# Performance work log

Hardware: AMD Instinct MI355X
Metric: run time of the kernel (lower is better)

The kernel has to match this reference:

```python
import jax, jax.numpy as jnp
import numpy as np

B, N, F, E, H, A, V, L = 128, 196, 512, 512, 512, 512, 30000, 21


def setup_inputs() -> dict:
    key = jax.random.key(0)
    ks = jax.random.split(key, 20)
    s = 0.02
    d = {
        "feats": jax.random.normal(ks[0], (B, N, F), jnp.float32),
        "captions": jax.random.randint(ks[1], (B, L), 1, V),
        "embed_W": (jax.random.normal(ks[2], (V, E), jnp.float32) * s).at[0].set(0.0),
        "Wf_w": jax.random.normal(ks[3], (A, F), jnp.float32) * s,
        "Wf_b": jnp.zeros((A,), jnp.float32),
        "Wh_w": jax.random.normal(ks[4], (A, H), jnp.float32) * s,
        "Wh_b": jnp.zeros((A,), jnp.float32),
        "v_w": jax.random.normal(ks[5], (1, A), jnp.float32) * s,
        "v_b": jnp.zeros((1,), jnp.float32),
        "W_ih": jax.random.normal(ks[6], (4 * H, E + F), jnp.float32) * s,
        "W_hh": jax.random.normal(ks[7], (4 * H, H), jnp.float32) * s,
        "b_ih": jnp.zeros((4 * H,), jnp.float32),
        "b_hh": jnp.zeros((4 * H,), jnp.float32),
        "init_w": jax.random.normal(ks[8], (H, F), jnp.float32) * s,
        "init_b": jnp.zeros((H,), jnp.float32),
        "initc_w": jax.random.normal(ks[9], (H, F), jnp.float32) * s,
        "initc_b": jnp.zeros((H,), jnp.float32),
        "out_w": jax.random.normal(ks[10], (V, H), jnp.float32) * s,
        "out_b": jnp.zeros((V,), jnp.float32),
    }
    return d


def reference(feats, captions, embed_W, Wf_w, Wf_b, Wh_w, Wh_b, v_w, v_b,
              W_ih, W_hh, b_ih, b_hh, init_w, init_b, initc_w, initc_b,
              out_w, out_b):
    # padding_idx=0 -> embedding row 0 is zero
    emW = embed_W.at[0].set(0.0)
    emb = emW[captions[:, :-1]]                       # [B, T, E], T = L-1
    gfeat = feats.mean(axis=1)                        # [B, F]
    h0 = gfeat @ init_w.T + init_b                    # [B, H]
    c0 = gfeat @ initc_w.T + initc_b                  # [B, H]
    # attention feature projection is timestep-invariant: hoist out of loop
    fproj = jnp.einsum('bnf,af->bna', feats, Wf_w) + Wf_b  # [B, N, A]

    def step(carry, emb_t):
        h, c = carry
        hproj = h @ Wh_w.T + Wh_b                     # [B, A]
        e = jnp.tanh(fproj + hproj[:, None, :])       # [B, N, A]
        scores = jnp.einsum('bna,a->bn', e, v_w[0]) + v_b[0]
        w = jax.nn.softmax(scores, axis=1)            # [B, N]
        ctx = jnp.einsum('bnf,bn->bf', feats, w)      # [B, F]
        x = jnp.concatenate([emb_t, ctx], axis=1)     # [B, E+F]
        gates = x @ W_ih.T + b_ih + h @ W_hh.T + b_hh # [B, 4H]
        i, f, g, o = jnp.split(gates, 4, axis=1)      # torch gate order i,f,g,o
        i = jax.nn.sigmoid(i)
        f = jax.nn.sigmoid(f)
        g = jnp.tanh(g)
        o = jax.nn.sigmoid(o)
        c = f * c + i * g
        h = o * jnp.tanh(c)
        logit = h @ out_w.T + out_b                   # [B, V]
        return (h, c), logit

    _, logits = jax.lax.scan(step, (h0, c0), jnp.swapaxes(emb, 0, 1))
    return jnp.swapaxes(logits, 0, 1)                 # [B, T, V]
```

## Files before the change

### kernel.cpp

```cpp
#include <hip/hip_runtime.h>
#include <stdint.h>
#include <stddef.h>

typedef unsigned short u16;
typedef __attribute__((ext_vector_type(8))) short short8;
typedef __attribute__((ext_vector_type(4))) float f32x4;

#define DEV static __device__ __forceinline__

DEV float bf2f(u16 u){ return __uint_as_float(((unsigned)u)<<16); }
DEV u16 f2bf(float f){ unsigned x=__float_as_uint(f); return (u16)((x + 0x7fffu + ((x>>16)&1u))>>16); }

DEV float wsum(float v){
#pragma unroll
  for(int o=32;o;o>>=1) v += __shfl_xor(v,o);
  return v;
}
DEV float wmax(float v){
#pragma unroll
  for(int o=32;o;o>>=1) v = fmaxf(v,__shfl_xor(v,o));
  return v;
}
DEV float sigm(float x){ return __fdividef(1.f, 1.f+__expf(-x)); }
DEV float tanhx(float x){ float e=__expf(-2.f*fabsf(x)); float t=__fdividef(1.f-e,1.f+e); return x<0.f?-t:t; }

DEV f32x4 mfma16(short8 a, short8 b, f32x4 c){
  asm("v_mfma_f32_16x16x32_bf16 %0, %1, %2, %0" : "+v"(c) : "v"(a), "v"(b));
  return c;
}
DEV void gll16(const void* g, void* l){
  __builtin_amdgcn_global_load_lds((const __attribute__((address_space(1))) void*)g,
                                   (__attribute__((address_space(3))) void*)l, 16, 0, 0);
}

DEV void pack8(u16* dst, const float* src){
  const float4 a=*(const float4*)(src);
  const float4 b=*(const float4*)(src+4);
  short8 o;
  o[0]=(short)f2bf(a.x); o[1]=(short)f2bf(a.y); o[2]=(short)f2bf(a.z); o[3]=(short)f2bf(a.w);
  o[4]=(short)f2bf(b.x); o[5]=(short)f2bf(b.y); o[6]=(short)f2bf(b.z); o[7]=(short)f2bf(b.w);
  *(short8*)dst=o;
}
DEV void zero8(u16* dst){
  short8 z;
#pragma unroll
  for(int e=0;e<8;++e) z[e]=0;
  *(short8*)dst=z;
}

__global__ __launch_bounds__(256) void setup_cast(
  const float* __restrict__ feats, const int* __restrict__ captions,
  const float* __restrict__ embW, const float* __restrict__ Wf_w,
  const float* __restrict__ Wh_w, const float* __restrict__ W_ih,
  const float* __restrict__ W_hh, const float* __restrict__ b_ih,
  const float* __restrict__ b_hh, const float* __restrict__ out_w,
  u16* __restrict__ feats_bf, u16* __restrict__ outw_bf, u16* __restrict__ Wc,
  u16* __restrict__ WihE, u16* __restrict__ embx, u16* __restrict__ Whw_bf,
  u16* __restrict__ Wf_bf, float* __restrict__ bias_comb)
{
  const long long o0=12845056LL,o1=28246016LL,o2=30343168LL,o3=31391744LL,
                  o4=32702464LL,o5=32964608LL,o6=33226752LL,total=33228800LL;
  for (long long i8=((long long)blockIdx.x*256+threadIdx.x)*8; i8<total;
       i8+=(long long)gridDim.x*256*8){
    const long long i=i8;
    if (i<o0){ pack8(feats_bf+i, feats+i); }
    else if (i<o1){ const long long j=i-o0; const int r=(int)(j>>9);
      if (r<30000) pack8(outw_bf+j, out_w+j); else zero8(outw_bf+j); }
    else if (i<o2){ const long long j=i-o1; const int r=(int)(j>>10), k=(int)(j&1023);
      const int o=((r&3)<<9)+(r>>2);
      const float* s=(k<512)? (W_ih+(size_t)o*1024+512+k) : (W_hh+(size_t)o*512+(k-512));
      pack8(Wc+j, s); }
    else if (i<o3){ const long long j=i-o2; const int r=(int)(j>>9), k=(int)(j&511);
      const int o=((r&3)<<9)+(r>>2);
      pack8(WihE+j, W_ih+(size_t)o*1024+k); }
    else if (i<o4){ const long long j=i-o3; const int m=(int)(j>>9), e=(int)(j&511);
      const int b=m/20, tt=m-b*20; const int idx=captions[b*21+tt];
      if (idx) pack8(embx+j, embW+(size_t)idx*512+e); else zero8(embx+j); }
    else if (i<o5){ const long long j=i-o4; pack8(Whw_bf+j, Wh_w+j); }
    else if (i<o6){ const long long j=i-o5; pack8(Wf_bf+j, Wf_w+j); }
    else { const long long j=i-o6;
      for(int e=0;e<8;++e){ const int r=(int)(j+e); const int o=((r&3)<<9)+(r>>2);
        bias_comb[r]=b_ih[o]+b_hh[o]; } }
  }
}

__global__ __launch_bounds__(256) void prep(
  const float* __restrict__ feats, const float* __restrict__ init_w,
  const float* __restrict__ init_b, const float* __restrict__ initc_w,
  const float* __restrict__ initc_b, u16* __restrict__ xs0, float* __restrict__ cbuf)
{
  const int b=blockIdx.x, tid=threadIdx.x, lane=tid&63, w=tid>>6;
  __shared__ float gf[512];
  const float* fb=feats+(size_t)b*196*512;
  float a0=0.f,a1=0.f;
  for(int n=0;n<196;++n){ a0+=fb[(size_t)n*512+tid]; a1+=fb[(size_t)n*512+tid+256]; }
  gf[tid]=a0*(1.f/196.f); gf[tid+256]=a1*(1.f/196.f);
  __syncthreads();
  const int kb=lane*8;
  float g8[8];
#pragma unroll
  for(int e=0;e<8;++e) g8[e]=gf[kb+e];
  for(int j=w*128;j<w*128+128;++j){
    const float* r1=init_w+(size_t)j*512+kb;
    const float* r2=initc_w+(size_t)j*512+kb;
    float s1=0.f,s2=0.f;
#pragma unroll
    for(int e=0;e<8;++e){ s1+=g8[e]*r1[e]; s2+=g8[e]*r2[e]; }
    s1=wsum(s1); s2=wsum(s2);
    if(lane==(j&63)){ xs0[b*1024+512+j]=f2bf(s1+init_b[j]); cbuf[b*512+j]=s2+initc_b[j]; }
  }
}

__global__ __launch_bounds__(1024) void attn_step(
  const u16* __restrict__ fproj, const u16* __restrict__ feats_bf,
  u16* __restrict__ xs, const u16* __restrict__ Whw,
  const float* __restrict__ Whb, const float* __restrict__ vw,
  const float* __restrict__ vb, const float* __restrict__ gemb,
  const float* __restrict__ gpart, float* __restrict__ cbuf,
  u16* __restrict__ h_all, int t)
{
  const int b=blockIdx.x, tid=threadIdx.x, lane=tid&63, w=tid>>6;
  __shared__ float part[16][512];
  __shared__ float hsf[512], hp[512], sc[208], red[16];
  if (t>0){
    if (tid<512){
      const int u=tid;
      float4 g4=*(const float4*)&gemb[((size_t)b*20+(t-1))*2048+u*4];
#pragma unroll
      for(int kz=0;kz<4;++kz){
        const float4 p=*(const float4*)&gpart[((size_t)kz*128+b)*2048+u*4];
        g4.x+=p.x; g4.y+=p.y; g4.z+=p.z; g4.w+=p.w;
      }
      const float cn=sigm(g4.y)*cbuf[b*512+u]+sigm(g4.x)*tanhx(g4.z);
      const float hn=sigm(g4.w)*tanhx(cn);
      cbuf[b*512+u]=cn;
      const u16 hb=f2bf(hn);
      xs[b*1024+512+u]=hb;
      h_all[((size_t)b*20+(t-1))*512+u]=hb;
      hsf[u]=bf2f(hb);
    }
  } else {
    if (tid<512) hsf[tid]=bf2f(xs[b*1024+512+tid]);
  }
  __syncthreads();
  const int kb=lane*8;
  float h8[8];
#pragma unroll
  for(int e=0;e<8;++e) h8[e]=hsf[kb+e];
  for(int jj=0;jj<32;jj+=2){
    const int j=w*32+jj;
    short8 w0=*(const short8*)(Whw+(size_t)j*512+kb);
    short8 w1=*(const short8*)(Whw+(size_t)(j+1)*512+kb);
    float s0=0.f,s1=0.f;
#pragma unroll
    for(int e=0;e<8;++e){
      s0+=h8[e]*bf2f((u16)w0[e]);
      s1+=h8[e]*bf2f((u16)w1[e]);
    }
    s0=wsum(s0); s1=wsum(s1);
    if(lane==0){ hp[j]=s0+Whb[j]; hp[j+1]=s1+Whb[j+1]; }
  }
  __syncthreads();
  float p2[8], vm2[8];
  float sv=0.f;
#pragma unroll
  for(int e=0;e<8;++e){
    const float p=hp[kb+e], v=vw[kb+e];
    p2[e]=2.f*p; vm2[e]=-2.f*v; sv+=v;
  }
  const float vb0=vb[0];
#pragma unroll
  for(int i=0;i<12;i+=2){
    const int n0=w+16*i, n1=n0+16;
    short8 f0=*(const short8*)(fproj+((size_t)b*196+n0)*512+kb);
    short8 f1=*(const short8*)(fproj+((size_t)b*196+n1)*512+kb);
    float s0=sv, s1=sv;
#pragma unroll
    for(int e=0;e<8;++e){
      const float x0=fmaf(bf2f((u16)f0[e]),2.f,p2[e]);
      const float x1=fmaf(bf2f((u16)f1[e]),2.f,p2[e]);
      s0+=__fdividef(vm2[e],__expf(x0)+1.f);
      s1+=__fdividef(vm2[e],__expf(x1)+1.f);
    }
    s0=wsum(s0); s1=wsum(s1);
    if(lane==0){ sc[n0]=s0+vb0; sc[n1]=s1+vb0; }
  }
  {
    const int n=w+192;
    if (n<196){
      short8 f0=*(const short8*)(fproj+((size_t)b*196+n)*512+kb);
      float s0=sv;
#pragma unroll
      for(int e=0;e<8;++e){
        const float x0=fmaf(bf2f((u16)f0[e]),2.f,p2[e]);
        s0+=__fdividef(vm2[e],__expf(x0)+1.f);
      }
      s0=wsum(s0);
      if(lane==0) sc[n]=s0+vb0;
    }
  }
  __syncthreads();
  float xv=(tid<196)? sc[tid] : -3.0e38f;
  float mx=wmax(xv);
  if(lane==0) red[w]=mx;
  __syncthreads();
  float mm=red[0];
#pragma unroll
  for(int i=1;i<16;++i) mm=fmaxf(mm,red[i]);
  float pv=(tid<196)? __expf(xv-mm) : 0.f;
  float ps=wsum(pv);
  __syncthreads();
  if(lane==0) red[w]=ps;
  __syncthreads();
  float tot=red[0];
#pragma unroll
  for(int i=1;i<16;++i) tot+=red[i];
  if(tid<196) sc[tid]=__fdividef(pv,tot);
  __syncthreads();
  float a8[8];
#pragma unroll
  for(int e=0;e<8;++e) a8[e]=0.f;
  for(int n=w;n<196;n+=16){
    short8 fv=*(const short8*)(feats_bf+((size_t)b*196+n)*512+kb);
    const float wn=sc[n];
#pragma unroll
    for(int e=0;e<8;++e) a8[e]+=wn*bf2f((u16)fv[e]);
  }
  *(float4*)&part[w][kb]  =*(float4*)&a8[0];
  *(float4*)&part[w][kb+4]=*(float4*)&a8[4];
  __syncthreads();
  if (tid<512){
    float s=0.f;
#pragma unroll
    for(int i=0;i<16;++i) s+=part[i][tid];
    xs[b*1024+tid]=f2bf(s);
  }
}

__global__ __launch_bounds__(512) void lstm_fin(
  const float* __restrict__ gemb, const float* __restrict__ gpart,
  const float* __restrict__ cbuf, u16* __restrict__ h_all)
{
  const int b=blockIdx.x, u=threadIdx.x;
  float4 g4=*(const float4*)&gemb[((size_t)b*20+19)*2048+u*4];
#pragma unroll
  for(int kz=0;kz<4;++kz){
    const float4 p=*(const float4*)&gpart[((size_t)kz*128+b)*2048+u*4];
    g4.x+=p.x; g4.y+=p.y; g4.z+=p.z; g4.w+=p.w;
  }
  const float cn=sigm(g4.y)*cbuf[b*512+u]+sigm(g4.x)*tanhx(g4.z);
  const float hn=sigm(g4.w)*tanhx(cn);
  h_all[((size_t)b*20+19)*512+u]=f2bf(hn);
}

template<int MODE>
__global__ __launch_bounds__(256) void gemm_bt(
  const u16* __restrict__ A, int lda, const u16* __restrict__ Bw, int ldb, int K,
  const float* __restrict__ bias, float* __restrict__ outf, u16* __restrict__ outb,
  int ncols)
{
  const int bm=(MODE==4)? 0 : blockIdx.y*128;
  const int kz=(MODE==4)? blockIdx.y : 0;
  const int bn=blockIdx.x*128;
  const u16* __restrict__ Ap=A +(size_t)kz*256;
  const u16* __restrict__ Bp=Bw+(size_t)kz*256;
  const int tid=threadIdx.x, lane=tid&63, wave=tid>>6;
  const int wr=(wave>>1)*64, wc=(wave&1)*64;
  __shared__ u16 As[128*32], Bs[128*32];
  f32x4 acc[4][4]={};
  const int srow=tid>>2, scol=(tid&3)*8;
  for(int k0=0;k0<K;k0+=32){
    gll16(Ap+(size_t)(bm+srow)*lda    +k0+scol, As+tid*8);
    gll16(Ap+(size_t)(bm+64+srow)*lda +k0+scol, As+2048+tid*8);
    gll16(Bp+(size_t)(bn+srow)*ldb    +k0+scol, Bs+tid*8);
    gll16(Bp+(size_t)(bn+64+srow)*ldb +k0+scol, Bs+2048+tid*8);
    __syncthreads();
    short8 af[4], bfr[4];
    const int ro=lane&15, ko=(lane>>4)*8;
#pragma unroll
    for(int m=0;m<4;++m) af[m]=*(const short8*)(As+(wr+m*16+ro)*32+ko);
#pragma unroll
    for(int n=0;n<4;++n) bfr[n]=*(const short8*)(Bs+(wc+n*16+ro)*32+ko);
#pragma unroll
    for(int m=0;m<4;++m)
#pragma unroll
      for(int n=0;n<4;++n) acc[m][n]=mfma16(af[m],bfr[n],acc[m][n]);
    __syncthreads();
  }
  asm volatile("s_nop 7\ns_nop 7\ns_nop 7");
  const int ro4=(lane>>4)*4, co=lane&15;
#pragma unroll
  for(int m=0;m<4;++m)
#pragma unroll
    for(int n=0;n<4;++n)
#pragma unroll
      for(int j=0;j<4;++j){
        const int r=bm+wr+m*16+ro4+j, c=bn+wc+n*16+co;
        if constexpr (MODE==0)      outb[(size_t)r*ncols+c]=f2bf(acc[m][n][j]+bias[c]);
        else if constexpr (MODE==1) outf[(size_t)r*ncols+c]=acc[m][n][j]+bias[c];
        else if constexpr (MODE==2){ if (c<ncols) outf[(size_t)r*ncols+c]=acc[m][n][j]+bias[c]; }
        else                        outf[((size_t)kz*128+r)*ncols+c]=acc[m][n][j];
      }
}

extern "C" void kernel_launch(void* const* d_in, const int* in_sizes, int n_in,
                              void* d_out, int out_size, void* d_ws, size_t ws_size,
                              hipStream_t stream) {
  const float* feats   =(const float*)d_in[0];
  const int*   captions=(const int*)  d_in[1];
  const float* embW    =(const float*)d_in[2];
  const float* Wf_w    =(const float*)d_in[3];
  const float* Wf_b    =(const float*)d_in[4];
  const float* Wh_w    =(const float*)d_in[5];
  const float* Wh_b    =(const float*)d_in[6];
  const float* v_w     =(const float*)d_in[7];
  const float* v_b     =(const float*)d_in[8];
  const float* W_ih    =(const float*)d_in[9];
  const float* W_hh    =(const float*)d_in[10];
  const float* b_ih    =(const float*)d_in[11];
  const float* b_hh    =(const float*)d_in[12];
  const float* init_w  =(const float*)d_in[13];
  const float* init_b  =(const float*)d_in[14];
  const float* initc_w =(const float*)d_in[15];
  const float* initc_b =(const float*)d_in[16];
  const float* out_w   =(const float*)d_in[17];
  const float* out_b   =(const float*)d_in[18];
  float* out=(float*)d_out;
  char* ws=(char*)d_ws;

  u16*   feats_bf =(u16*)  (ws+0);
  u16*   fproj    =(u16*)  (ws+25690112);
  u16*   outw_bf  =(u16*)  (ws+51380224);
  u16*   Wc       =(u16*)  (ws+82182144);
  u16*   WihE     =(u16*)  (ws+86376448);
  u16*   Whw_bf   =(u16*)  (ws+88473600);
  u16*   Wf_bf    =(u16*)  (ws+88997888);
  u16*   embx     =(u16*)  (ws+89522176);
  u16*   h_all    =(u16*)  (ws+92143616);
  u16*   xs0      =(u16*)  (ws+94765056);
  float* gemb     =(float*)(ws+95289344);
  float* cbuf     =(float*)(ws+116260864);
  float* bias_comb=(float*)(ws+116523008);
  float* gpart    =(float*)(ws+116531200);

  setup_cast<<<4096,256,0,stream>>>(feats,captions,embW,Wf_w,Wh_w,W_ih,W_hh,b_ih,b_hh,out_w,
                                    feats_bf,outw_bf,Wc,WihE,embx,Whw_bf,Wf_bf,bias_comb);
  prep<<<128,256,0,stream>>>(feats,init_w,init_b,initc_w,initc_b,xs0,cbuf);
  gemm_bt<0><<<dim3(4,196),256,0,stream>>>(feats_bf,512,Wf_bf,512,512,
      Wf_b,nullptr,fproj,512);
  gemm_bt<1><<<dim3(16,20),256,0,stream>>>(embx,512,WihE,512,512,
      bias_comb,gemb,nullptr,2048);

  for(int t=0;t<20;++t){
    attn_step<<<128,1024,0,stream>>>(fproj,feats_bf,xs0,Whw_bf,Wh_b,v_w,v_b,
                                     gemb,gpart,cbuf,h_all,t);
    gemm_bt<4><<<dim3(16,4),256,0,stream>>>(xs0,1024,Wc,1024,256,
        nullptr,gpart,nullptr,2048);
  }
  lstm_fin<<<128,512,0,stream>>>(gemb,gpart,cbuf,h_all);
  gemm_bt<2><<<dim3(235,20),256,0,stream>>>(h_all,512,outw_bf,512,512,
      out_b,out,nullptr,30000);
}
```

Measured before the change: 1.245 ms.

## Fuse recurrent timestep loop into one persistent kernel with grid barriers

Replaces the 20 pairs of attention and recurrent-GEMM launches plus the final LSTM kernel with a single persistent 128-block kernel that loops over timesteps. Blocks synchronise through a software grid barrier built on global atomics. The recurrent GEMM is redistributed so that each block computes a 128x128 tile with a split-K of 8 instead of 4. This removes about 40 launch boundaries, at the cost of two spin-wait grid barriers per step and a larger shared-memory footprint. It also relies on all 128 blocks being co-resident, which a plain launch does not guarantee.

```diff
diff --git a/kernel.cpp b/kernel.cpp
--- a/kernel.cpp
+++ b/kernel.cpp
@@ -46,6 +46,25 @@
 #pragma unroll
   for(int e=0;e<8;++e) z[e]=0;
   *(short8*)dst=z;
+}
+
+DEV void gbar(unsigned* cnt, unsigned* gen, int nblk){
+  __syncthreads();
+  if (threadIdx.x==0){
+    __threadfence();
+    unsigned g=__hip_atomic_load(gen,__ATOMIC_RELAXED,__HIP_MEMORY_SCOPE_AGENT);
+    unsigned a=__hip_atomic_fetch_add(cnt,1u,__ATOMIC_ACQ_REL,__HIP_MEMORY_SCOPE_AGENT);
+    if (a==(unsigned)(nblk-1)){
+      __hip_atomic_store(cnt,0u,__ATOMIC_RELAXED,__HIP_MEMORY_SCOPE_AGENT);
+      __hip_atomic_store(gen,g+1u,__ATOMIC_RELEASE,__HIP_MEMORY_SCOPE_AGENT);
+    } else {
+      while(__hip_atomic_load(gen,__ATOMIC_ACQUIRE,__HIP_MEMORY_SCOPE_AGENT)==g){
+        __builtin_amdgcn_s_sleep(1);
+      }
+    }
+    __threadfence();
+  }
+  __syncthreads();
 }
 
 __global__ __launch_bounds__(256) void setup_cast(
@@ -111,146 +130,189 @@
   }
 }
 
-__global__ __launch_bounds__(1024) void attn_step(
+__global__ __launch_bounds__(1024) void megastep(
   const u16* __restrict__ fproj, const u16* __restrict__ feats_bf,
   u16* __restrict__ xs, const u16* __restrict__ Whw,
   const float* __restrict__ Whb, const float* __restrict__ vw,
   const float* __restrict__ vb, const float* __restrict__ gemb,
-  const float* __restrict__ gpart, float* __restrict__ cbuf,
-  u16* __restrict__ h_all, int t)
+  float* __restrict__ gpart, float* __restrict__ cbuf,
+  u16* __restrict__ h_all, const u16* __restrict__ Wc,
+  unsigned* __restrict__ bar)
 {
-  const int b=blockIdx.x, tid=threadIdx.x, lane=tid&63, w=tid>>6;
+  const int blk=blockIdx.x, tid=threadIdx.x, lane=tid&63, w=tid>>6;
+  const int b=blk;
   __shared__ float part[16][512];
   __shared__ float hsf[512], hp[512], sc[208], red[16];
-  if (t>0){
-    if (tid<512){
-      const int u=tid;
-      float4 g4=*(const float4*)&gemb[((size_t)b*20+(t-1))*2048+u*4];
-#pragma unroll
-      for(int kz=0;kz<4;++kz){
-        const float4 p=*(const float4*)&gpart[((size_t)kz*128+b)*2048+u*4];
-        g4.x+=p.x; g4.y+=p.y; g4.z+=p.z; g4.w+=p.w;
-      }
-      const float cn=sigm(g4.y)*cbuf[b*512+u]+sigm(g4.x)*tanhx(g4.z);
-      const float hn=sigm(g4.w)*tanhx(cn);
-      cbuf[b*512+u]=cn;
-      const u16 hb=f2bf(hn);
-      xs[b*1024+512+u]=hb;
-      h_all[((size_t)b*20+(t-1))*512+u]=hb;
-      hsf[u]=bf2f(hb);
-    }
-  } else {
-    if (tid<512) hsf[tid]=bf2f(xs[b*1024+512+tid]);
-  }
-  __syncthreads();
+  __shared__ u16 As[128*128], Bs[128*128];
+  unsigned* cnt=bar; unsigned* gen=bar+1;
+
   const int kb=lane*8;
-  float h8[8];
-#pragma unroll
-  for(int e=0;e<8;++e) h8[e]=hsf[kb+e];
-  for(int jj=0;jj<32;jj+=2){
-    const int j=w*32+jj;
-    short8 w0=*(const short8*)(Whw+(size_t)j*512+kb);
-    short8 w1=*(const short8*)(Whw+(size_t)(j+1)*512+kb);
-    float s0=0.f,s1=0.f;
+  const int kz=blk>>4, nt=blk&15;
+
+  for (int t=0;t<20;++t){
+    if (t>0){
+      if (tid<512){
+        const int u=tid;
+        float4 g4=*(const float4*)&gemb[((size_t)b*20+(t-1))*2048+u*4];
+#pragma unroll
+        for(int z=0;z<8;++z){
+          const float4 p=*(const float4*)&gpart[((size_t)z*128+b)*2048+u*4];
+          g4.x+=p.x; g4.y+=p.y; g4.z+=p.z; g4.w+=p.w;
+        }
+        const float cn=sigm(g4.y)*cbuf[b*512+u]+sigm(g4.x)*tanhx(g4.z);
+        const float hn=sigm(g4.w)*tanhx(cn);
+        cbuf[b*512+u]=cn;
+        const u16 hb=f2bf(hn);
+        xs[b*1024+512+u]=hb;
+        h_all[((size_t)b*20+(t-1))*512+u]=hb;
+        hsf[u]=bf2f(hb);
+      }
+    } else {
+      if (tid<512) hsf[tid]=bf2f(xs[b*1024+512+tid]);
+    }
+    __syncthreads();
+    float h8[8];
+#pragma unroll
+    for(int e=0;e<8;++e) h8[e]=hsf[kb+e];
+    for(int jj=0;jj<32;jj+=2){
+      const int j=w*32+jj;
+      short8 w0=*(const short8*)(Whw+(size_t)j*512+kb);
+      short8 w1=*(const short8*)(Whw+(size_t)(j+1)*512+kb);
+      float s0=0.f,s1=0.f;
+#pragma unroll
+      for(int e=0;e<8;++e){
+        s0+=h8[e]*bf2f((u16)w0[e]);
+        s1+=h8[e]*bf2f((u16)w1[e]);
+      }
+      s0=wsum(s0); s1=wsum(s1);
+      if(lane==0){ hp[j]=s0+Whb[j]; hp[j+1]=s1+Whb[j+1]; }
+    }
+    __syncthreads();
+    float p2[8], vm2[8];
+    float sv=0.f;
 #pragma unroll
     for(int e=0;e<8;++e){
-      s0+=h8[e]*bf2f((u16)w0[e]);
-      s1+=h8[e]*bf2f((u16)w1[e]);
-    }
-    s0=wsum(s0); s1=wsum(s1);
-    if(lane==0){ hp[j]=s0+Whb[j]; hp[j+1]=s1+Whb[j+1]; }
-  }
-  __syncthreads();
-  float p2[8], vm2[8];
-  float sv=0.f;
-#pragma unroll
-  for(int e=0;e<8;++e){
-    const float p=hp[kb+e], v=vw[kb+e];
-    p2[e]=2.f*p; vm2[e]=-2.f*v; sv+=v;
-  }
-  const float vb0=vb[0];
-#pragma unroll
-  for(int i=0;i<12;i+=2){
-    const int n0=w+16*i, n1=n0+16;
-    short8 f0=*(const short8*)(fproj+((size_t)b*196+n0)*512+kb);
-    short8 f1=*(const short8*)(fproj+((size_t)b*196+n1)*512+kb);
-    float s0=sv, s1=sv;
-#pragma unroll
-    for(int e=0;e<8;++e){
-      const float x0=fmaf(bf2f((u16)f0[e]),2.f,p2[e]);
-      const float x1=fmaf(bf2f((u16)f1[e]),2.f,p2[e]);
-      s0+=__fdividef(vm2[e],__expf(x0)+1.f);
-      s1+=__fdividef(vm2[e],__expf(x1)+1.f);
-    }
-    s0=wsum(s0); s1=wsum(s1);
-    if(lane==0){ sc[n0]=s0+vb0; sc[n1]=s1+vb0; }
-  }
-  {
-    const int n=w+192;
-    if (n<196){
-      short8 f0=*(const short8*)(fproj+((size_t)b*196+n)*512+kb);
-      float s0=sv;
+      const float p=hp[kb+e], v=vw[kb+e];
+      p2[e]=2.f*p; vm2[e]=-2.f*v; sv+=v;
+    }
+    const float vb0=vb[0];
+#pragma unroll
+    for(int i=0;i<12;i+=2){
+      const int n0=w+16*i, n1=n0+16;
+      short8 f0=*(const short8*)(fproj+((size_t)b*196+n0)*512+kb);
+      short8 f1=*(const short8*)(fproj+((size_t)b*196+n1)*512+kb);
+      float s0=sv, s1=sv;
 #pragma unroll
       for(int e=0;e<8;++e){
         const float x0=fmaf(bf2f((u16)f0[e]),2.f,p2[e]);
+        const float x1=fmaf(bf2f((u16)f1[e]),2.f,p2[e]);
         s0+=__fdividef(vm2[e],__expf(x0)+1.f);
-      }
-      s0=wsum(s0);
-      if(lane==0) sc[n]=s0+vb0;
-    }
-  }
-  __syncthreads();
-  float xv=(tid<196)? sc[tid] : -3.0e38f;
-  float mx=wmax(xv);
-  if(lane==0) red[w]=mx;
-  __syncthreads();
-  float mm=red[0];
-#pragma unroll
-  for(int i=1;i<16;++i) mm=fmaxf(mm,red[i]);
-  float pv=(tid<196)? __expf(xv-mm) : 0.f;
-  float ps=wsum(pv);
-  __syncthreads();
-  if(lane==0) red[w]=ps;
-  __syncthreads();
-  float tot=red[0];
-#pragma unroll
-  for(int i=1;i<16;++i) tot+=red[i];
-  if(tid<196) sc[tid]=__fdividef(pv,tot);
-  __syncthreads();
-  float a8[8];
-#pragma unroll
-  for(int e=0;e<8;++e) a8[e]=0.f;
-  for(int n=w;n<196;n+=16){
-    short8 fv=*(const short8*)(feats_bf+((size_t)b*196+n)*512+kb);
-    const float wn=sc[n];
-#pragma unroll
-    for(int e=0;e<8;++e) a8[e]+=wn*bf2f((u16)fv[e]);
-  }
-  *(float4*)&part[w][kb]  =*(float4*)&a8[0];
-  *(float4*)&part[w][kb+4]=*(float4*)&a8[4];
-  __syncthreads();
+        s1+=__fdividef(vm2[e],__expf(x1)+1.f);
+      }
+      s0=wsum(s0); s1=wsum(s1);
+      if(lane==0){ sc[n0]=s0+vb0; sc[n1]=s1+vb0; }
+    }
+    {
+      const int n=w+192;
+      if (n<196){
+        short8 f0=*(const short8*)(fproj+((size_t)b*196+n)*512+kb);
+        float s0=sv;
+#pragma unroll
+        for(int e=0;e<8;++e){
+          const float x0=fmaf(bf2f((u16)f0[e]),2.f,p2[e]);
+          s0+=__fdividef(vm2[e],__expf(x0)+1.f);
+        }
+        s0=wsum(s0);
+        if(lane==0) sc[n]=s0+vb0;
+      }
+    }
+    __syncthreads();
+    float xv=(tid<196)? sc[tid] : -3.0e38f;
+    float mx=wmax(xv);
+    if(lane==0) red[w]=mx;
+    __syncthreads();
+    float mm=red[0];
+#pragma unroll
+    for(int i=1;i<16;++i) mm=fmaxf(mm,red[i]);
+    float pv=(tid<196)? __expf(xv-mm) : 0.f;
+    float ps=wsum(pv);
+    __syncthreads();
+    if(lane==0) red[w]=ps;
+    __syncthreads();
+    float tot=red[0];
+#pragma unroll
+    for(int i=1;i<16;++i) tot+=red[i];
+    if(tid<196) sc[tid]=__fdividef(pv,tot);
+    __syncthreads();
+    float a8[8];
+#pragma unroll
+    for(int e=0;e<8;++e) a8[e]=0.f;
+    for(int n=w;n<196;n+=16){
+      short8 fv=*(const short8*)(feats_bf+((size_t)b*196+n)*512+kb);
+      const float wn=sc[n];
+#pragma unroll
+      for(int e=0;e<8;++e) a8[e]+=wn*bf2f((u16)fv[e]);
+    }
+    *(float4*)&part[w][kb]  =*(float4*)&a8[0];
+    *(float4*)&part[w][kb+4]=*(float4*)&a8[4];
+    __syncthreads();
+    if (tid<512){
+      float s=0.f;
+#pragma unroll
+      for(int i=0;i<16;++i) s+=part[i][tid];
+      xs[b*1024+tid]=f2bf(s);
+    }
+
+    gbar(cnt,gen,128);
+
+#pragma unroll
+    for(int i=0;i<2;++i){
+      const int idx=i*1024+tid;
+      gll16(xs+(size_t)(idx>>4)*1024 + kz*128 + (idx&15)*8, As+idx*8);
+    }
+#pragma unroll
+    for(int i=0;i<2;++i){
+      const int idx=i*1024+tid;
+      gll16(Wc+(size_t)(nt*128+(idx>>4))*1024 + kz*128 + (idx&15)*8, Bs+idx*8);
+    }
+    __syncthreads();
+    {
+      f32x4 acc[4]={};
+      const int mf=w>>1, nc0=(w&1)*64, ro=lane&15, ko=(lane>>4)*8;
+#pragma unroll
+      for(int kk=0;kk<4;++kk){
+        short8 af=*(const short8*)(As+(size_t)(mf*16+ro)*128+kk*32+ko);
+#pragma unroll
+        for(int n=0;n<4;++n){
+          short8 bfv=*(const short8*)(Bs+(size_t)(nc0+n*16+ro)*128+kk*32+ko);
+          acc[n]=mfma16(af,bfv,acc[n]);
+        }
+      }
+      asm volatile("s_nop 7\ns_nop 7\ns_nop 7");
+      const int ro4=(lane>>4)*4, co=lane&15;
+#pragma unroll
+      for(int n=0;n<4;++n)
+#pragma unroll
+        for(int j=0;j<4;++j){
+          const int r=mf*16+ro4+j, c=nt*128+nc0+n*16+co;
+          gpart[((size_t)kz*128+r)*2048+c]=acc[n][j];
+        }
+    }
+    gbar(cnt,gen,128);
+  }
+
   if (tid<512){
-    float s=0.f;
-#pragma unroll
-    for(int i=0;i<16;++i) s+=part[i][tid];
-    xs[b*1024+tid]=f2bf(s);
-  }
-}
-
-__global__ __launch_bounds__(512) void lstm_fin(
-  const float* __restrict__ gemb, const float* __restrict__ gpart,
-  const float* __restrict__ cbuf, u16* __restrict__ h_all)
-{
-  const int b=blockIdx.x, u=threadIdx.x;
-  float4 g4=*(const float4*)&gemb[((size_t)b*20+19)*2048+u*4];
-#pragma unroll
-  for(int kz=0;kz<4;++kz){
-    const float4 p=*(const float4*)&gpart[((size_t)kz*128+b)*2048+u*4];
-    g4.x+=p.x; g4.y+=p.y; g4.z+=p.z; g4.w+=p.w;
-  }
-  const float cn=sigm(g4.y)*cbuf[b*512+u]+sigm(g4.x)*tanhx(g4.z);
-  const float hn=sigm(g4.w)*tanhx(cn);
-  h_all[((size_t)b*20+19)*512+u]=f2bf(hn);
+    const int u=tid;
+    float4 g4=*(const float4*)&gemb[((size_t)b*20+19)*2048+u*4];
+#pragma unroll
+    for(int z=0;z<8;++z){
+      const float4 p=*(const float4*)&gpart[((size_t)z*128+b)*2048+u*4];
+      g4.x+=p.x; g4.y+=p.y; g4.z+=p.z; g4.w+=p.w;
+    }
+    const float cn=sigm(g4.y)*cbuf[b*512+u]+sigm(g4.x)*tanhx(g4.z);
+    const float hn=sigm(g4.w)*tanhx(cn);
+    h_all[((size_t)b*20+19)*512+u]=f2bf(hn);
+  }
 }
 
 template<int MODE>
@@ -259,21 +321,17 @@
   const float* __restrict__ bias, float* __restrict__ outf, u16* __restrict__ outb,
   int ncols)
 {
-  const int bm=(MODE==4)? 0 : blockIdx.y*128;
-  const int kz=(MODE==4)? blockIdx.y : 0;
-  const int bn=blockIdx.x*128;
-  const u16* __restrict__ Ap=A +(size_t)kz*256;
-  const u16* __restrict__ Bp=Bw+(size_t)kz*256;
+  const int bm=blockIdx.y*128, bn=blockIdx.x*128;
   const int tid=threadIdx.x, lane=tid&63, wave=tid>>6;
   const int wr=(wave>>1)*64, wc=(wave&1)*64;
   __shared__ u16 As[128*32], Bs[128*32];
   f32x4 acc[4][4]={};
   const int srow=tid>>2, scol=(tid&3)*8;
   for(int k0=0;k0<K;k0+=32){
-    gll16(Ap+(size_t)(bm+srow)*lda    +k0+scol, As+tid*8);
-    gll16(Ap+(size_t)(bm+64+srow)*lda +k0+scol, As+2048+tid*8);
-    gll16(Bp+(size_t)(bn+srow)*ldb    +k0+scol, Bs+tid*8);
-    gll16(Bp+(size_t)(bn+64+srow)*ldb +k0+scol, Bs+2048+tid*8);
+    gll16(A +(size_t)(bm+srow)*lda    +k0+scol, As+tid*8);
+    gll16(A +(size_t)(bm+64+srow)*lda +k0+scol, As+2048+tid*8);
+    gll16(Bw+(size_t)(bn+srow)*ldb    +k0+scol, Bs+tid*8);
+    gll16(Bw+(size_t)(bn+64+srow)*ldb +k0+scol, Bs+2048+tid*8);
     __syncthreads();
     short8 af[4], bfr[4];
     const int ro=lane&15, ko=(lane>>4)*8;
@@ -298,8 +356,7 @@
         const int r=bm+wr+m*16+ro4+j, c=bn+wc+n*16+co;
         if constexpr (MODE==0)      outb[(size_t)r*ncols+c]=f2bf(acc[m][n][j]+bias[c]);
         else if constexpr (MODE==1) outf[(size_t)r*ncols+c]=acc[m][n][j]+bias[c];
-        else if constexpr (MODE==2){ if (c<ncols) outf[(size_t)r*ncols+c]=acc[m][n][j]+bias[c]; }
-        else                        outf[((size_t)kz*128+r)*ncols+c]=acc[m][n][j];
+        else { if (c<ncols) outf[(size_t)r*ncols+c]=acc[m][n][j]+bias[c]; }
       }
 }
 
@@ -342,7 +399,9 @@
   float* cbuf     =(float*)(ws+116260864);
   float* bias_comb=(float*)(ws+116523008);
   float* gpart    =(float*)(ws+116531200);
-
+  unsigned* bar   =(unsigned*)(ws+126000000);
+
+  hipMemsetAsync(bar, 0, 8, stream);
   setup_cast<<<4096,256,0,stream>>>(feats,captions,embW,Wf_w,Wh_w,W_ih,W_hh,b_ih,b_hh,out_w,
                                     feats_bf,outw_bf,Wc,WihE,embx,Whw_bf,Wf_bf,bias_comb);
   prep<<<128,256,0,stream>>>(feats,init_w,init_b,initc_w,initc_b,xs0,cbuf);
@@ -351,13 +410,9 @@
   gemm_bt<1><<<dim3(16,20),256,0,stream>>>(embx,512,WihE,512,512,
       bias_comb,gemb,nullptr,2048);
 
-  for(int t=0;t<20;++t){
-    attn_step<<<128,1024,0,stream>>>(fproj,feats_bf,xs0,Whw_bf,Wh_b,v_w,v_b,
-                                     gemb,gpart,cbuf,h_all,t);
-    gemm_bt<4><<<dim3(16,4),256,0,stream>>>(xs0,1024,Wc,1024,256,
-        nullptr,gpart,nullptr,2048);
-  }
-  lstm_fin<<<128,512,0,stream>>>(gemb,gpart,cbuf,h_all);
+  megastep<<<128,1024,0,stream>>>(fproj,feats_bf,xs0,Whw_bf,Wh_b,v_w,v_b,
+                                  gemb,gpart,cbuf,h_all,Wc,bar);
+
   gemm_bt<2><<<dim3(235,20),256,0,stream>>>(h_all,512,outw_bf,512,512,
       out_b,out,nullptr,30000);
 }
```

Measured after the change: 3.504 ms. +181.5%, slower.

## Split attention step into score and context kernels over two blocks per batch

Applied to the files above, without the earlier changes.

The per-batch 1024-thread attention kernel becomes two 512-thread kernels, each launched with two blocks per batch row. Each block owns half the attention positions or half the context features, so the 128-row recurrence fills more CUs. Scores now go through a global buffer and the cell state is double-buffered, because both half-blocks recompute the LSTM update and Wh projection redundantly. The output-projection GEMM grid is also transposed so consecutive blocks share the same weight tile, improving cache reuse. The price is an extra kernel launch per timestep plus duplicated projection work.

```diff
diff --git a/kernel.cpp b/kernel.cpp
--- a/kernel.cpp
+++ b/kernel.cpp
@@ -4,6 +4,7 @@
 
 typedef unsigned short u16;
 typedef __attribute__((ext_vector_type(8))) short short8;
+typedef __attribute__((ext_vector_type(4))) short short4v;
 typedef __attribute__((ext_vector_type(4))) float f32x4;
 
 #define DEV static __device__ __forceinline__
@@ -111,44 +112,43 @@
   }
 }
 
-__global__ __launch_bounds__(1024) void attn_step(
-  const u16* __restrict__ fproj, const u16* __restrict__ feats_bf,
-  u16* __restrict__ xs, const u16* __restrict__ Whw,
-  const float* __restrict__ Whb, const float* __restrict__ vw,
-  const float* __restrict__ vb, const float* __restrict__ gemb,
-  const float* __restrict__ gpart, float* __restrict__ cbuf,
-  u16* __restrict__ h_all, int t)
-{
-  const int b=blockIdx.x, tid=threadIdx.x, lane=tid&63, w=tid>>6;
-  __shared__ float part[16][512];
-  __shared__ float hsf[512], hp[512], sc[208], red[16];
+__global__ __launch_bounds__(512) void attn_sc(
+  const u16* __restrict__ fproj, u16* __restrict__ xs,
+  const u16* __restrict__ Whw, const float* __restrict__ Whb,
+  const float* __restrict__ vw, const float* __restrict__ vb,
+  const float* __restrict__ gemb, const float* __restrict__ gpart,
+  float* __restrict__ cbuf, u16* __restrict__ h_all,
+  float* __restrict__ sc_g, int t)
+{
+  const int blk=blockIdx.x, tid=threadIdx.x, lane=tid&63, w=tid>>6;
+  const int b=blk>>1, h=blk&1;
+  __shared__ float hsf[512], hp[512];
   if (t>0){
-    if (tid<512){
-      const int u=tid;
-      float4 g4=*(const float4*)&gemb[((size_t)b*20+(t-1))*2048+u*4];
-#pragma unroll
-      for(int kz=0;kz<4;++kz){
-        const float4 p=*(const float4*)&gpart[((size_t)kz*128+b)*2048+u*4];
-        g4.x+=p.x; g4.y+=p.y; g4.z+=p.z; g4.w+=p.w;
-      }
-      const float cn=sigm(g4.y)*cbuf[b*512+u]+sigm(g4.x)*tanhx(g4.z);
-      const float hn=sigm(g4.w)*tanhx(cn);
-      cbuf[b*512+u]=cn;
-      const u16 hb=f2bf(hn);
-      xs[b*1024+512+u]=hb;
-      h_all[((size_t)b*20+(t-1))*512+u]=hb;
-      hsf[u]=bf2f(hb);
-    }
+    const int u=tid;
+    float4 g4=*(const float4*)&gemb[((size_t)b*20+(t-1))*2048+u*4];
+#pragma unroll
+    for(int kz=0;kz<4;++kz){
+      const float4 p=*(const float4*)&gpart[((size_t)kz*128+b)*2048+u*4];
+      g4.x+=p.x; g4.y+=p.y; g4.z+=p.z; g4.w+=p.w;
+    }
+    const float cold=cbuf[((t-1)&1)*65536 + b*512+u];
+    const float cn=sigm(g4.y)*cold+sigm(g4.x)*tanhx(g4.z);
+    const float hn=sigm(g4.w)*tanhx(cn);
+    cbuf[(t&1)*65536 + b*512+u]=cn;
+    const u16 hb=f2bf(hn);
+    xs[b*1024+512+u]=hb;
+    h_all[((size_t)b*20+(t-1))*512+u]=hb;
+    hsf[u]=bf2f(hb);
   } else {
-    if (tid<512) hsf[tid]=bf2f(xs[b*1024+512+tid]);
+    hsf[tid]=bf2f(xs[b*1024+512+tid]);
   }
   __syncthreads();
   const int kb=lane*8;
   float h8[8];
 #pragma unroll
   for(int e=0;e<8;++e) h8[e]=hsf[kb+e];
-  for(int jj=0;jj<32;jj+=2){
-    const int j=w*32+jj;
+  for(int jj=0;jj<64;jj+=2){
+    const int j=w*64+jj;
     short8 w0=*(const short8*)(Whw+(size_t)j*512+kb);
     short8 w1=*(const short8*)(Whw+(size_t)(j+1)*512+kb);
     float s0=0.f,s1=0.f;
@@ -169,71 +169,98 @@
     p2[e]=2.f*p; vm2[e]=-2.f*v; sv+=v;
   }
   const float vb0=vb[0];
-#pragma unroll
-  for(int i=0;i<12;i+=2){
-    const int n0=w+16*i, n1=n0+16;
-    short8 f0=*(const short8*)(fproj+((size_t)b*196+n0)*512+kb);
-    short8 f1=*(const short8*)(fproj+((size_t)b*196+n1)*512+kb);
-    float s0=sv, s1=sv;
+  const int base=h*98;
+#pragma unroll
+  for(int i=0;i<12;i+=4){
+    const int n0=base+w+8*i;
+    short8 f0=*(const short8*)(fproj+((size_t)b*196+n0   )*512+kb);
+    short8 f1=*(const short8*)(fproj+((size_t)b*196+n0+8 )*512+kb);
+    short8 f2=*(const short8*)(fproj+((size_t)b*196+n0+16)*512+kb);
+    short8 f3=*(const short8*)(fproj+((size_t)b*196+n0+24)*512+kb);
+    float s0=sv,s1=sv,s2=sv,s3=sv;
 #pragma unroll
     for(int e=0;e<8;++e){
-      const float x0=fmaf(bf2f((u16)f0[e]),2.f,p2[e]);
-      const float x1=fmaf(bf2f((u16)f1[e]),2.f,p2[e]);
-      s0+=__fdividef(vm2[e],__expf(x0)+1.f);
-      s1+=__fdividef(vm2[e],__expf(x1)+1.f);
-    }
-    s0=wsum(s0); s1=wsum(s1);
-    if(lane==0){ sc[n0]=s0+vb0; sc[n1]=s1+vb0; }
+      s0+=__fdividef(vm2[e],__expf(fmaf(bf2f((u16)f0[e]),2.f,p2[e]))+1.f);
+      s1+=__fdividef(vm2[e],__expf(fmaf(bf2f((u16)f1[e]),2.f,p2[e]))+1.f);
+      s2+=__fdividef(vm2[e],__expf(fmaf(bf2f((u16)f2[e]),2.f,p2[e]))+1.f);
+      s3+=__fdividef(vm2[e],__expf(fmaf(bf2f((u16)f3[e]),2.f,p2[e]))+1.f);
+    }
+    s0=wsum(s0); s1=wsum(s1); s2=wsum(s2); s3=wsum(s3);
+    if(lane==0){
+      sc_g[b*224+n0   ]=s0+vb0;
+      sc_g[b*224+n0+8 ]=s1+vb0;
+      sc_g[b*224+n0+16]=s2+vb0;
+      sc_g[b*224+n0+24]=s3+vb0;
+    }
+  }
+  if (w<2){
+    const int n=base+96+w;
+    short8 f0=*(const short8*)(fproj+((size_t)b*196+n)*512+kb);
+    float s0=sv;
+#pragma unroll
+    for(int e=0;e<8;++e)
+      s0+=__fdividef(vm2[e],__expf(fmaf(bf2f((u16)f0[e]),2.f,p2[e]))+1.f);
+    s0=wsum(s0);
+    if(lane==0) sc_g[b*224+n]=s0+vb0;
+  }
+}
+
+__global__ __launch_bounds__(512) void ctx_step(
+  const u16* __restrict__ feats_bf, u16* __restrict__ xs,
+  const float* __restrict__ sc_g)
+{
+  const int blk=blockIdx.x, tid=threadIdx.x, lane=tid&63, w=tid>>6;
+  const int b=blk>>1, h=blk&1;
+  __shared__ float scw[208], red[8];
+  __shared__ float part[8][256];
+  float xv=(tid<196)? sc_g[b*224+tid] : -3.0e38f;
+  float mx=wmax(xv);
+  if(lane==0) red[w]=mx;
+  __syncthreads();
+  float mm=red[0];
+#pragma unroll
+  for(int i=1;i<8;++i) mm=fmaxf(mm,red[i]);
+  float pv=(tid<196)? __expf(xv-mm) : 0.f;
+  float ps=wsum(pv);
+  __syncthreads();
+  if(lane==0) red[w]=ps;
+  __syncthreads();
+  float tot=red[0];
+#pragma unroll
+  for(int i=1;i<8;++i) tot+=red[i];
+  if(tid<196) scw[tid]=__fdividef(pv,tot);
+  __syncthreads();
+  float4 acc; acc.x=0.f; acc.y=0.f; acc.z=0.f; acc.w=0.f;
+  const int cb=h*256+lane*4;
+#pragma unroll
+  for(int i=0;i<24;i+=2){
+    const int n0=w+8*i, n1=n0+8;
+    short4v v0=*(const short4v*)(feats_bf+((size_t)b*196+n0)*512+cb);
+    short4v v1=*(const short4v*)(feats_bf+((size_t)b*196+n1)*512+cb);
+    const float w0=scw[n0], w1=scw[n1];
+    acc.x+=w0*bf2f((u16)v0[0])+w1*bf2f((u16)v1[0]);
+    acc.y+=w0*bf2f((u16)v0[1])+w1*bf2f((u16)v1[1]);
+    acc.z+=w0*bf2f((u16)v0[2])+w1*bf2f((u16)v1[2]);
+    acc.w+=w0*bf2f((u16)v0[3])+w1*bf2f((u16)v1[3]);
   }
   {
     const int n=w+192;
     if (n<196){
-      short8 f0=*(const short8*)(fproj+((size_t)b*196+n)*512+kb);
-      float s0=sv;
-#pragma unroll
-      for(int e=0;e<8;++e){
-        const float x0=fmaf(bf2f((u16)f0[e]),2.f,p2[e]);
-        s0+=__fdividef(vm2[e],__expf(x0)+1.f);
-      }
-      s0=wsum(s0);
-      if(lane==0) sc[n]=s0+vb0;
-    }
-  }
-  __syncthreads();
-  float xv=(tid<196)? sc[tid] : -3.0e38f;
-  float mx=wmax(xv);
-  if(lane==0) red[w]=mx;
-  __syncthreads();
-  float mm=red[0];
-#pragma unroll
-  for(int i=1;i<16;++i) mm=fmaxf(mm,red[i]);
-  float pv=(tid<196)? __expf(xv-mm) : 0.f;
-  float ps=wsum(pv);
-  __syncthreads();
-  if(lane==0) red[w]=ps;
-  __syncthreads();
-  float tot=red[0];
-#pragma unroll
-  for(int i=1;i<16;++i) tot+=red[i];
-  if(tid<196) sc[tid]=__fdividef(pv,tot);
-  __syncthreads();
-  float a8[8];
-#pragma unroll
-  for(int e=0;e<8;++e) a8[e]=0.f;
-  for(int n=w;n<196;n+=16){
-    short8 fv=*(const short8*)(feats_bf+((size_t)b*196+n)*512+kb);
-    const float wn=sc[n];
-#pragma unroll
-    for(int e=0;e<8;++e) a8[e]+=wn*bf2f((u16)fv[e]);
-  }
-  *(float4*)&part[w][kb]  =*(float4*)&a8[0];
-  *(float4*)&part[w][kb+4]=*(float4*)&a8[4];
-  __syncthreads();
-  if (tid<512){
+      short4v v0=*(const short4v*)(feats_bf+((size_t)b*196+n)*512+cb);
+      const float w0=scw[n];
+      acc.x+=w0*bf2f((u16)v0[0]);
+      acc.y+=w0*bf2f((u16)v0[1]);
+      acc.z+=w0*bf2f((u16)v0[2]);
+      acc.w+=w0*bf2f((u16)v0[3]);
+    }
+  }
+  *(float4*)&part[w][lane*4]=acc;
+  __syncthreads();
+  if (tid<256){
     float s=0.f;
 #pragma unroll
-    for(int i=0;i<16;++i) s+=part[i][tid];
-    xs[b*1024+tid]=f2bf(s);
+    for(int i=0;i<8;++i) s+=part[i][tid];
+    xs[b*1024 + h*256 + tid]=f2bf(s);
   }
 }
 
@@ -248,7 +275,7 @@
     const float4 p=*(const float4*)&gpart[((size_t)kz*128+b)*2048+u*4];
     g4.x+=p.x; g4.y+=p.y; g4.z+=p.z; g4.w+=p.w;
   }
-  const float cn=sigm(g4.y)*cbuf[b*512+u]+sigm(g4.x)*tanhx(g4.z);
+  const float cn=sigm(g4.y)*cbuf[65536 + b*512+u]+sigm(g4.x)*tanhx(g4.z);
   const float hn=sigm(g4.w)*tanhx(cn);
   h_all[((size_t)b*20+19)*512+u]=f2bf(hn);
 }
@@ -259,9 +286,9 @@
   const float* __restrict__ bias, float* __restrict__ outf, u16* __restrict__ outb,
   int ncols)
 {
-  const int bm=(MODE==4)? 0 : blockIdx.y*128;
+  const int bm=(MODE==4)? 0 : ((MODE==2)? blockIdx.x*128 : blockIdx.y*128);
+  const int bn=(MODE==2)? blockIdx.y*128 : blockIdx.x*128;
   const int kz=(MODE==4)? blockIdx.y : 0;
-  const int bn=blockIdx.x*128;
   const u16* __restrict__ Ap=A +(size_t)kz*256;
   const u16* __restrict__ Bp=Bw+(size_t)kz*256;
   const int tid=threadIdx.x, lane=tid&63, wave=tid>>6;
@@ -340,8 +367,9 @@
   u16*   xs0      =(u16*)  (ws+94765056);
   float* gemb     =(float*)(ws+95289344);
   float* cbuf     =(float*)(ws+116260864);
-  float* bias_comb=(float*)(ws+116523008);
-  float* gpart    =(float*)(ws+116531200);
+  float* bias_comb=(float*)(ws+116785152);
+  float* gpart    =(float*)(ws+116793344);
+  float* sc_g     =(float*)(ws+120987648);
 
   setup_cast<<<4096,256,0,stream>>>(feats,captions,embW,Wf_w,Wh_w,W_ih,W_hh,b_ih,b_hh,out_w,
                                     feats_bf,outw_bf,Wc,WihE,embx,Whw_bf,Wf_bf,bias_comb);
@@ -352,12 +380,13 @@
       bias_comb,gemb,nullptr,2048);
 
   for(int t=0;t<20;++t){
-    attn_step<<<128,1024,0,stream>>>(fproj,feats_bf,xs0,Whw_bf,Wh_b,v_w,v_b,
-                                     gemb,gpart,cbuf,h_all,t);
+    attn_sc<<<256,512,0,stream>>>(fproj,xs0,Whw_bf,Wh_b,v_w,v_b,
+                                  gemb,gpart,cbuf,h_all,sc_g,t);
+    ctx_step<<<256,512,0,stream>>>(feats_bf,xs0,sc_g);
     gemm_bt<4><<<dim3(16,4),256,0,stream>>>(xs0,1024,Wc,1024,256,
         nullptr,gpart,nullptr,2048);
   }
   lstm_fin<<<128,512,0,stream>>>(gemb,gpart,cbuf,h_all);
-  gemm_bt<2><<<dim3(235,20),256,0,stream>>>(h_all,512,outw_bf,512,512,
+  gemm_bt<2><<<dim3(20,235),256,0,stream>>>(h_all,512,outw_bf,512,512,
       out_b,out,nullptr,30000);
 }
```

After: 1.342 ms. +7.8%, slower.
